# Performance work log

Measured on AMD Instinct MI355X. Metric: run time of the kernel, lower is better.

## Reference

```python
import jax, jax.numpy as jnp
import numpy as np

N, IN_DIM, HIDDEN = 10000, 512, 128
EPS = 1e-12  # torch F.normalize eps


def setup_inputs() -> dict:
    key = jax.random.key(0)
    k1, k2 = jax.random.split(key, 2)
    feat = jax.random.normal(k1, (N, IN_DIM), dtype=jnp.float32)
    W = jax.random.normal(k2, (IN_DIM, HIDDEN), dtype=jnp.float32) * 0.02
    b = jnp.zeros((HIDDEN,), dtype=jnp.float32)
    return {"feat": feat, "W": W, "b": b, "k": 15}


def reference(feat, W, b, k):
    # Linear projection: z = feat @ W + b  -> [N, H]
    z = feat @ W + b
    # L2-normalize rows (F.normalize with eps clamp)
    norm = jnp.maximum(jnp.linalg.norm(z, axis=-1, keepdims=True), EPS)
    z = z / norm
    # Dense cosine similarity matrix [N, N]
    sim = z @ z.T
    n = sim.shape[0]
    kk = min(k, n - 1)
    # Top-k neighbors per row
    _, topk_idx = jax.lax.top_k(sim, kk)  # [N, kk] int32
    rows = jnp.arange(n)
    mask = jnp.zeros_like(sim).at[rows[:, None], topk_idx].set(1.0)
    # Zero the diagonal (fill_diagonal_(0.0))
    mask = mask.at[rows, rows].set(0.0)
    return sim * mask
```

## Files before the change

### kernel.cpp

```cpp
#include <hip/hip_runtime.h>
#include <hip/hip_bf16.h>
#include <math.h>
#include <float.h>

#define NROWS  10000
#define INDIM  512
#define KSPLIT 384
#define HID    128
#define NSTRIP 8
#define STRIPW 1250
#define CHUNK  64
#define NCHUNK 20
#define CAPS   96
#define RESC   32
#define KOUT   14
#define ZPADR  10112
#define GRIDX  79
#define NBLK   632
#define Z4TOT  25000000
#define Z4BLK  39557
#define Z4CHK  1978
#define C_TAU  2.05f

using short8 = __attribute__((ext_vector_type(8))) short;
using f32x4  = __attribute__((ext_vector_type(4))) float;

__global__ __launch_bounds__(128)
void k_projnorm(const float* __restrict__ feat, const float* __restrict__ W,
                const float* __restrict__ b, float* __restrict__ z32,
                __hip_bfloat16* __restrict__ zb) {
    const int h = threadIdx.x;
    const int row0 = blockIdx.x * 8;
    if (row0 >= NROWS) {
#pragma unroll
        for (int r = 0; r < 8; ++r)
            if (row0 + r < ZPADR) zb[(size_t)(row0 + r) * HID + h] = __float2bfloat16(0.f);
        return;
    }
    __shared__ float fl[8][INDIM];
#pragma unroll
    for (int i = 0; i < 8; ++i)
        *(float4*)&fl[i][h * 4] = *(const float4*)(feat + (size_t)(row0 + i) * INDIM + h * 4);
    __syncthreads();

    float accA[8], accB[8];
#pragma unroll
    for (int r = 0; r < 8; ++r) { accA[r] = 0.f; accB[r] = 0.f; }
#pragma unroll 4
    for (int k4 = 0; k4 < 96; ++k4) {
        const int k = k4 * 4;
        const float w0 = W[(k + 0) * HID + h];
        const float w1 = W[(k + 1) * HID + h];
        const float w2 = W[(k + 2) * HID + h];
        const float w3 = W[(k + 3) * HID + h];
#pragma unroll
        for (int r = 0; r < 8; ++r) {
            const float4 f = *(const float4*)&fl[r][k];
            accA[r] = fmaf(f.x, w0, accA[r]);
            accA[r] = fmaf(f.y, w1, accA[r]);
            accA[r] = fmaf(f.z, w2, accA[r]);
            accA[r] = fmaf(f.w, w3, accA[r]);
        }
    }
#pragma unroll 4
    for (int k4 = 96; k4 < 128; ++k4) {
        const int k = k4 * 4;
        const float w0 = W[(k + 0) * HID + h];
        const float w1 = W[(k + 1) * HID + h];
        const float w2 = W[(k + 2) * HID + h];
        const float w3 = W[(k + 3) * HID + h];
#pragma unroll
        for (int r = 0; r < 8; ++r) {
            const float4 f = *(const float4*)&fl[r][k];
            accB[r] = fmaf(f.x, w0, accB[r]);
            accB[r] = fmaf(f.y, w1, accB[r]);
            accB[r] = fmaf(f.z, w2, accB[r]);
            accB[r] = fmaf(f.w, w3, accB[r]);
        }
    }
    __shared__ float zl[8][HID];
    __shared__ float nrm[8];
    const float bh = b[h];
#pragma unroll
    for (int r = 0; r < 8; ++r)
        zl[r][h] = __fadd_rn(__fadd_rn(accA[r], accB[r]), bh);
    __syncthreads();
    if (h < 8) {
        float rr[8];
#pragma unroll
        for (int j = 0; j < 8; ++j) rr[j] = __fmul_rn(zl[h][j], zl[h][j]);
        for (int i = 8; i < HID; i += 8)
#pragma unroll
            for (int j = 0; j < 8; ++j)
                rr[j] = __fadd_rn(rr[j], __fmul_rn(zl[h][i + j], zl[h][i + j]));
        const float s = __fadd_rn(
            __fadd_rn(__fadd_rn(rr[0], rr[1]), __fadd_rn(rr[2], rr[3])),
            __fadd_rn(__fadd_rn(rr[4], rr[5]), __fadd_rn(rr[6], rr[7])));
        nrm[h] = fmaxf(__fsqrt_rn(s), 1e-12f);
    }
    __syncthreads();
#pragma unroll
    for (int r = 0; r < 8; ++r) {
        const float v = __fdiv_rn(zl[r][h], nrm[r]);
        z32[(size_t)(row0 + r) * HID + h] = v;
        zb [(size_t)(row0 + r) * HID + h] = __float2bfloat16(v);
    }
}

__global__ __launch_bounds__(512)
void k_cand(const __hip_bfloat16* __restrict__ zbp, f32x4* __restrict__ out4,
            int* __restrict__ cnt4, unsigned int* __restrict__ list) {
    __shared__ ushort Bt[2][8192];
    __shared__ int lcnt[128];
    const char* zbb = (const char*)zbp;
    const int tid = threadIdx.x, lane = tid & 63, wid = tid >> 6;
    const int row0 = blockIdx.x * 128;
    const int strip = blockIdx.y;
    const int jbase = strip * STRIPW;
    const int bid = strip * GRIDX + blockIdx.x;
    const int row_g = row0 + wid * 16 + (lane & 15);
    const int rloc  = wid * 16 + (lane & 15);
    const int swz = (lane & 7) << 4;

    if (tid < 128) lcnt[tid] = 0;

    short8 afr[4];
    {
        const char* ap = zbb + (size_t)row_g * 256 + ((lane >> 4) * 16);
        afr[0] = *(const short8*)(ap);
        afr[1] = *(const short8*)(ap + 64);
        afr[2] = *(const short8*)(ap + 128);
        afr[3] = *(const short8*)(ap + 192);
    }

    const int sjl = tid >> 3;
    const int sir = (tid & 7) * 32;
    const int sw0 = sir ^ ((sjl & 7) << 4);
    const int sw1 = (sir + 16) ^ ((sjl & 7) << 4);

    {
        const char* src = zbb + (size_t)(jbase + sjl) * 256 + sir;
        const uint4 d0 = *(const uint4*)(src);
        const uint4 d1 = *(const uint4*)(src + 16);
        char* dst = (char*)Bt[0] + (size_t)sjl * 256;
        *(uint4*)(dst + sw0) = d0;
        *(uint4*)(dst + sw1) = d1;
    }
    __syncthreads();

    const size_t zb0 = (size_t)bid * Z4BLK;
    int zlen = Z4TOT - (int)zb0; if (zlen > Z4BLK) zlen = Z4BLK;
    f32x4* zp = out4 + zb0;
    const f32x4 zero4 = {0.f, 0.f, 0.f, 0.f};

    float ss = 0.f;

#pragma unroll 1
    for (int c = 0; c < NCHUNK; ++c) {
        const int jc = c * CHUNK;
        const char* cur = (const char*)Bt[c & 1];

        uint4 st0, st1;
        const bool nx = (c + 1 < NCHUNK);
        if (nx) {
            const char* src = zbb + (size_t)(jbase + jc + CHUNK + sjl) * 256 + sir;
            st0 = *(const uint4*)(src);
            st1 = *(const uint4*)(src + 16);
        }

        {
            const int z0 = c * Z4CHK;
            int ze = z0 + Z4CHK; if (ze > zlen) ze = zlen;
            for (int i = z0 + tid; i < ze; i += 512)
                __builtin_nontemporal_store(zero4, zp + i);
        }

        float tau;
        if (c == 0) tau = 0.10f;
        else {
            const float n = 64.f * (float)c;
            const float w = 1.f - 3.f * __frsqrt_rn(2.f * n);
            tau = fmaxf(C_TAU * w * __fsqrt_rn(ss / n), 0.08f);
        }

        f32x4 acc[4];
#pragma unroll
        for (int t = 0; t < 4; ++t) {
            acc[t] = (f32x4){0.f, 0.f, 0.f, 0.f};
            const char* rp = cur + (size_t)(t * 16 + (lane & 15)) * 256;
#pragma unroll
            for (int ks = 0; ks < 4; ++ks) {
                const short8 bfr = *(const short8*)(rp + ((ks * 64 + (lane >> 4) * 16) ^ swz));
                acc[t] = __builtin_amdgcn_mfma_f32_16x16x32_bf16(bfr, afr[ks], acc[t], 0, 0, 0);
            }
        }

        float ssl = 0.f;
#pragma unroll
        for (int t = 0; t < 4; ++t) {
#pragma unroll
            for (int r = 0; r < 4; ++r) {
                const float val = acc[t][r];
                const int js = jc + t * 16 + ((lane >> 4) << 2) + r;
                const int jg = jbase + js;
                const bool ok = (js < STRIPW) && (jg != row_g);
                ssl += ok ? val * val : 0.f;
                if (ok && val > tau) {
                    const unsigned int u = __builtin_bit_cast(unsigned int, val);
                    const unsigned int pk = (((u + 0x8000u) >> 16) << 16) | (unsigned int)jg;
                    const int pos = atomicAdd(&lcnt[rloc], 1);
                    if (pos < CAPS)
                        list[((size_t)row_g * NSTRIP + strip) * CAPS + pos] = pk;
                }
            }
        }
        ssl += __shfl_xor(ssl, 16, 64);
        ssl += __shfl_xor(ssl, 32, 64);
        ss += ssl;

        if (nx) {
            char* wb = (char*)Bt[(c + 1) & 1] + (size_t)sjl * 256;
            *(uint4*)(wb + sw0) = st0;
            *(uint4*)(wb + sw1) = st1;
        }
        __syncthreads();
    }

    if (tid < 128) {
        const int row = row0 + tid;
        if (row < NROWS) cnt4[row * NSTRIP + strip] = lcnt[tid];
    }
}

#define CEK(a, b) { const unsigned int x_ = k[a], y_ = k[b]; \
    k[a] = x_ > y_ ? x_ : y_; k[b] = x_ > y_ ? y_ : x_; }

__global__ __launch_bounds__(256)
void k_select(const float* __restrict__ z32, const int* __restrict__ cnt4,
              const unsigned int* __restrict__ list, float* __restrict__ out) {
    __shared__ float zr[4][HID];
    const int tid = threadIdx.x, wid = tid >> 6, lane = tid & 63;
    const int row = blockIdx.x * 4 + wid;

    *(float2*)&zr[wid][lane * 2] = *(const float2*)(z32 + (size_t)row * HID + lane * 2);
    __syncthreads();

    unsigned int k[16];
#pragma unroll
    for (int t = 0; t < 12; ++t) {
        const int p = t * 64 + lane;
        const int seg = p / CAPS;
        const int off = p - seg * CAPS;
        int cn = cnt4[row * NSTRIP + seg]; if (cn > CAPS) cn = CAPS;
        k[t] = (off < cn) ? list[((size_t)row * NSTRIP + seg) * CAPS + off] : 0u;
    }
#pragma unroll
    for (int t = 12; t < 16; ++t) k[t] = 0u;

#pragma unroll
    for (int size = 2; size <= 16; size <<= 1) {
#pragma unroll
        for (int stride = size >> 1; stride > 0; stride >>= 1) {
#pragma unroll
            for (int i = 0; i < 16; ++i) {
                const int j = i ^ stride;
                if (j > i) {
                    if ((i & size) == 0) { CEK(i, j); } else { CEK(j, i); }
                }
            }
        }
    }

    unsigned int win = 0u;
#pragma unroll 1
    for (int t = 0; t < RESC; ++t) {
        unsigned int m = k[0];
#pragma unroll
        for (int msk = 1; msk <= 32; msk <<= 1) {
            const unsigned int o = (unsigned int)__shfl_xor((int)m, msk, 64);
            m = o > m ? o : m;
        }
        if (lane == t) win = m;
        if (k[0] == m && m != 0u) {
#pragma unroll
            for (int s = 0; s < 15; ++s) k[s] = k[s + 1];
            k[15] = 0u;
        }
    }

    float ex = -INFINITY; int idx = 0x7fffffff;
    const bool act = (lane < RESC) && (win != 0u);
    if (act) {
        idx = (int)(win & 0xFFFFu);
        const float* p = z32 + (size_t)idx * HID;
        float a = 0.f;
#pragma unroll
        for (int k4 = 0; k4 < 32; ++k4) {
            const float4 bb = *(const float4*)(p + k4 * 4);
            const float4 zz = *(const float4*)&zr[wid][k4 * 4];
            a = fmaf(zz.x, bb.x, a);
            a = fmaf(zz.y, bb.y, a);
            a = fmaf(zz.z, bb.z, a);
            a = fmaf(zz.w, bb.w, a);
        }
        ex = a;
    }

    bool alive = act;
#pragma unroll 1
    for (int t = 0; t < KOUT; ++t) {
        float mv = alive ? ex : -INFINITY;
        int   mi = alive ? idx : 0x7fffffff;
#pragma unroll
        for (int msk = 1; msk <= 32; msk <<= 1) {
            const float ov = __shfl_xor(mv, msk, 64);
            const int   oj = __shfl_xor(mi, msk, 64);
            const bool take = (ov > mv) || (ov == mv && oj < mi);
            mv = take ? ov : mv; mi = take ? oj : mi;
        }
        if (alive && idx == mi) {
            out[(size_t)row * NROWS + mi] = ex;
            alive = false;
        }
    }
}

extern "C" void kernel_launch(void* const* d_in, const int* in_sizes, int n_in,
                              void* d_out, int out_size, void* d_ws, size_t ws_size,
                              hipStream_t stream) {
    const float* feat = (const float*)d_in[0];
    const float* W    = (const float*)d_in[1];
    const float* b    = (const float*)d_in[2];
    float* out = (float*)d_out;

    char* ws = (char*)d_ws;
    float*          z32  = (float*)ws;
    __hip_bfloat16* zb   = (__hip_bfloat16*)(ws + 5120000);
    int*            cnt4 = (int*)(ws + 7708672);
    unsigned int*   lst  = (unsigned int*)(ws + 8028672);

    hipLaunchKernelGGL(k_projnorm, dim3(1264),          dim3(128), 0, stream, feat, W, b, z32, zb);
    hipLaunchKernelGGL(k_cand,     dim3(GRIDX, NSTRIP), dim3(512), 0, stream, zb, (f32x4*)out, cnt4, lst);
    hipLaunchKernelGGL(k_select,   dim3(2500),          dim3(256), 0, stream, z32, cnt4, lst, out);
}
```

Baseline: 239.4 us.

## Defer threshold pass after barrier and batch per-lane LDS atomics

The candidate-filter loop now writes the next B tile and hits the barrier before scanning the MFMA results, so the threshold scan and list writes can overlap with other waves. The reduction of the sum of squares and the tau update move to the start of the next chunk, which keeps the same tau sequence. Each lane now does one LDS atomicAdd per chunk covering all its passing values instead of one atomic per value. __syncthreads is replaced by an explicit lgkmcnt wait plus s_barrier, and a final barrier is added before the counts are read.

```diff
diff --git a/kernel.cpp b/kernel.cpp
--- a/kernel.cpp
+++ b/kernel.cpp
@@ -25,6 +25,11 @@
 using short8 = __attribute__((ext_vector_type(8))) short;
 using f32x4  = __attribute__((ext_vector_type(4))) float;
 
+__device__ __forceinline__ void lds_barrier() {
+    asm volatile("s_waitcnt lgkmcnt(0)" ::: "memory");
+    __builtin_amdgcn_s_barrier();
+}
+
 __global__ __launch_bounds__(128)
 void k_projnorm(const float* __restrict__ feat, const float* __restrict__ W,
                 const float* __restrict__ b, float* __restrict__ z32,
@@ -121,6 +126,7 @@
     const int row_g = row0 + wid * 16 + (lane & 15);
     const int rloc  = wid * 16 + (lane & 15);
     const int swz = (lane & 7) << 4;
+    const size_t segbase = ((size_t)row_g * NSTRIP + strip) * CAPS;
 
     if (tid < 128) lcnt[tid] = 0;
 
@@ -146,7 +152,7 @@
         *(uint4*)(dst + sw0) = d0;
         *(uint4*)(dst + sw1) = d1;
     }
-    __syncthreads();
+    lds_barrier();
 
     const size_t zb0 = (size_t)bid * Z4BLK;
     int zlen = Z4TOT - (int)zb0; if (zlen > Z4BLK) zlen = Z4BLK;
@@ -154,11 +160,25 @@
     const f32x4 zero4 = {0.f, 0.f, 0.f, 0.f};
 
     float ss = 0.f;
+    float ssl_p = 0.f;
 
 #pragma unroll 1
     for (int c = 0; c < NCHUNK; ++c) {
         const int jc = c * CHUNK;
         const char* cur = (const char*)Bt[c & 1];
+
+        {
+            float t1 = ssl_p + __shfl_xor(ssl_p, 16, 64);
+            t1 += __shfl_xor(t1, 32, 64);
+            ss += t1;
+        }
+        float tau;
+        if (c == 0) tau = 0.10f;
+        else {
+            const float n = 64.f * (float)c;
+            const float w = 1.f - 3.f * __frsqrt_rn(2.f * n);
+            tau = fmaxf(C_TAU * w * __fsqrt_rn(ss / n), 0.08f);
+        }
 
         uint4 st0, st1;
         const bool nx = (c + 1 < NCHUNK);
@@ -175,14 +195,6 @@
                 __builtin_nontemporal_store(zero4, zp + i);
         }
 
-        float tau;
-        if (c == 0) tau = 0.10f;
-        else {
-            const float n = 64.f * (float)c;
-            const float w = 1.f - 3.f * __frsqrt_rn(2.f * n);
-            tau = fmaxf(C_TAU * w * __fsqrt_rn(ss / n), 0.08f);
-        }
-
         f32x4 acc[4];
 #pragma unroll
         for (int t = 0; t < 4; ++t) {
@@ -195,37 +207,58 @@
             }
         }
 
-        float ssl = 0.f;
-#pragma unroll
-        for (int t = 0; t < 4; ++t) {
-#pragma unroll
-            for (int r = 0; r < 4; ++r) {
-                const float val = acc[t][r];
-                const int js = jc + t * 16 + ((lane >> 4) << 2) + r;
-                const int jg = jbase + js;
-                const bool ok = (js < STRIPW) && (jg != row_g);
-                ssl += ok ? val * val : 0.f;
-                if (ok && val > tau) {
-                    const unsigned int u = __builtin_bit_cast(unsigned int, val);
-                    const unsigned int pk = (((u + 0x8000u) >> 16) << 16) | (unsigned int)jg;
-                    const int pos = atomicAdd(&lcnt[rloc], 1);
-                    if (pos < CAPS)
-                        list[((size_t)row_g * NSTRIP + strip) * CAPS + pos] = pk;
-                }
-            }
-        }
-        ssl += __shfl_xor(ssl, 16, 64);
-        ssl += __shfl_xor(ssl, 32, 64);
-        ss += ssl;
-
         if (nx) {
             char* wb = (char*)Bt[(c + 1) & 1] + (size_t)sjl * 256;
             *(uint4*)(wb + sw0) = st0;
             *(uint4*)(wb + sw1) = st1;
         }
-        __syncthreads();
-    }
-
+        lds_barrier();
+
+        {
+            float ssl = 0.f;
+            unsigned int pm = 0u;
+            int np = 0;
+#pragma unroll
+            for (int t = 0; t < 4; ++t) {
+#pragma unroll
+                for (int r = 0; r < 4; ++r) {
+                    const int s = t * 4 + r;
+                    const float val = acc[t][r];
+                    const int js = jc + t * 16 + ((lane >> 4) << 2) + r;
+                    const int jg = jbase + js;
+                    const bool ok = (js < STRIPW) && (jg != row_g);
+                    ssl += ok ? val * val : 0.f;
+                    const bool pass = ok && (val > tau);
+                    pm |= pass ? (1u << s) : 0u;
+                    np += pass ? 1 : 0;
+                }
+            }
+            int base = 0;
+            if (np) base = atomicAdd(&lcnt[rloc], np);
+            if (pm) {
+#pragma unroll
+                for (int t = 0; t < 4; ++t) {
+#pragma unroll
+                    for (int r = 0; r < 4; ++r) {
+                        const int s = t * 4 + r;
+                        if ((pm >> s) & 1u) {
+                            if (base < CAPS) {
+                                const float val = acc[t][r];
+                                const unsigned int u = __builtin_bit_cast(unsigned int, val);
+                                const int jg = jbase + jc + t * 16 + ((lane >> 4) << 2) + r;
+                                list[segbase + base] =
+                                    (((u + 0x8000u) >> 16) << 16) | (unsigned int)jg;
+                            }
+                            ++base;
+                        }
+                    }
+                }
+            }
+            ssl_p = ssl;
+        }
+    }
+
+    lds_barrier();
     if (tid < 128) {
         const int row = row0 + tid;
         if (row < NROWS) cnt4[row * NSTRIP + strip] = lcnt[tid];
```

Result: no change. 243.6 us (+1.7%).
